# Optimization experiments

Measured on AMD Instinct MI355X. Metric: run time of the kernel, lower is better.

The kernel has to match this reference:

```python
import jax, jax.numpy as jnp
import numpy as np

EPS = 1e-12  # matches torch F.normalize default eps
TEMP = 0.1


def _gram(x):
    # L2-normalize rows; for unit vectors 1 - 0.5*||xi-xj||^2 == xi . xj
    n = x / jnp.maximum(jnp.linalg.norm(x, axis=-1, keepdims=True), EPS)
    return n @ n.T  # [N, N]


def setup_inputs() -> dict:
    key = jax.random.key(0)
    k1, k2, k3, k4 = jax.random.split(key, 4)
    N, D = 4096, 512
    return {
        "fm_rgb": jax.random.normal(k1, (N, D), dtype=jnp.float32),
        "fm_depth": jax.random.normal(k2, (N, D), dtype=jnp.float32),
        "fm_ir": jax.random.normal(k3, (N, D), dtype=jnp.float32),
        "fm_t": jax.random.normal(k4, (N, D), dtype=jnp.float32),
    }


def reference(fm_rgb, fm_depth, fm_ir, fm_t):
    G_rgb = _gram(fm_rgb)
    G_depth = _gram(fm_depth)
    G_ir = _gram(fm_ir)
    G_t = _gram(fm_t)
    inv_t = 1.0 / TEMP
    loss_rgb = jnp.mean((G_t * inv_t - G_rgb * inv_t) ** 2)
    loss_depth = jnp.mean((G_t * inv_t - G_depth * inv_t) ** 2)
    loss_ir = jnp.mean((G_t * inv_t - G_ir * inv_t) ** 2)
    return loss_rgb + loss_depth + loss_ir
```

## Files before the change

kernel.cpp:

```cpp
#include <hip/hip_runtime.h>
#include <hip/hip_bf16.h>


typedef __attribute__((ext_vector_type(4))) float floatx4;
typedef __attribute__((ext_vector_type(8))) unsigned short ushort8;

#define N_ROWS 4096
#define DDIM   512
#define NT8_BYTES    ((size_t)4 * DDIM * N_ROWS)
#define SLICE_FLOATS ((size_t)112 * 16384)
#define NSPLIT 4
#define LOSS_SCALE 9.094947017729282e-11f

__device__ __forceinline__ const float* sel_mod(int mod, const float* a,
                                                const float* b, const float* c,
                                                const float* d) {
  return mod == 0 ? a : mod == 1 ? b : mod == 2 ? c : d;
}

__global__ __launch_bounds__(256) void preprocess_kernel(
    const float* __restrict__ in0, const float* __restrict__ in1,
    const float* __restrict__ in2, const float* __restrict__ in3,
    unsigned char* __restrict__ nT8) {
  int mod = blockIdx.y;
  int k0 = blockIdx.x * 64;
  const float* X = sel_mod(mod, in0, in1, in2, in3) + (size_t)k0 * DDIM;

  __shared__ float rsc[64];
  __shared__ unsigned short tile[128][72];

  int t = threadIdx.x;
  int w = t >> 6, lane = t & 63;

#pragma unroll
  for (int i = 0; i < 16; ++i) {
    int r = w * 16 + i;
    const float4* rp = (const float4*)(X + (size_t)r * DDIM);
    float4 a = rp[lane];
    float4 b = rp[lane + 64];
    float ss = a.x * a.x + a.y * a.y + a.z * a.z + a.w * a.w +
               b.x * b.x + b.y * b.y + b.z * b.z + b.w * b.w;
#pragma unroll
    for (int off = 32; off > 0; off >>= 1) ss += __shfl_down(ss, off, 64);
    if (lane == 0) rsc[r] = 16.0f / fmaxf(sqrtf(ss), 1e-12f);
  }
  __syncthreads();

  for (int p = 0; p < 4; ++p) {
#pragma unroll
    for (int it = 0; it < 8; ++it) {
      int idx = it * 256 + t;
      int r = idx >> 5;
      int c4 = idx & 31;
      float4 v = ((const float4*)(X + (size_t)r * DDIM + p * 128))[c4];
      float sc = rsc[r];
      __hip_bfloat16 h0 = __float2bfloat16(v.x * sc);
      __hip_bfloat16 h1 = __float2bfloat16(v.y * sc);
      __hip_bfloat16 h2 = __float2bfloat16(v.z * sc);
      __hip_bfloat16 h3 = __float2bfloat16(v.w * sc);
      tile[c4 * 4 + 0][r] = *(unsigned short*)&h0;
      tile[c4 * 4 + 1][r] = *(unsigned short*)&h1;
      tile[c4 * 4 + 2][r] = *(unsigned short*)&h2;
      tile[c4 * 4 + 3][r] = *(unsigned short*)&h3;
    }
    __syncthreads();
#pragma unroll
    for (int it = 0; it < 2; ++it) {
      int idx = it * 256 + t;
      int c = idx >> 2;
      int g = idx & 3;
      ushort8 u0 = *(const ushort8*)&tile[c][g * 16];
      ushort8 u1 = *(const ushort8*)&tile[c][g * 16 + 8];
      float f[16];
#pragma unroll
      for (int j = 0; j < 8; ++j) {
        f[j] = __uint_as_float(((unsigned int)(unsigned short)u0[j]) << 16);
        f[8 + j] = __uint_as_float(((unsigned int)(unsigned short)u1[j]) << 16);
      }
      unsigned int wds[4];
#pragma unroll
      for (int q = 0; q < 4; ++q) {
        unsigned int pk = __builtin_amdgcn_cvt_pk_fp8_f32(f[4 * q], f[4 * q + 1], 0, 0);
        pk = __builtin_amdgcn_cvt_pk_fp8_f32(f[4 * q + 2], f[4 * q + 3], pk, 1);
        wds[q] = pk;
      }
      uint4 out = {wds[0], wds[1], wds[2], wds[3]};
      *(uint4*)(nT8 + ((size_t)(mod * DDIM + p * 128 + c)) * N_ROWS + k0 +
                g * 16) = out;
    }
    __syncthreads();
  }
}

__device__ __forceinline__ void stage_tiles(
    const unsigned char* __restrict__ Abase,
    const unsigned char* __restrict__ Bbase, int k0,
    unsigned char* lsA, unsigned char* lsB, int wave, int lane) {
  int rr = lane >> 3;
  int s = lane & 7;
#pragma unroll
  for (int c = 0; c < 4; ++c) {
    int base = wave * 32 + c * 8;
    int row = base + rr;
    int gc = s ^ ((row >> 1) & 7);
    const unsigned char* ga = Abase + (size_t)row * N_ROWS + k0 + gc * 16;
    const unsigned char* gb = Bbase + (size_t)row * N_ROWS + k0 + gc * 16;
    __builtin_amdgcn_global_load_lds(
        (__attribute__((address_space(1))) void*)(void*)ga,
        (__attribute__((address_space(3))) void*)(void*)&lsA[base * 128],
        16, 0, 0);
    __builtin_amdgcn_global_load_lds(
        (__attribute__((address_space(1))) void*)(void*)gb,
        (__attribute__((address_space(3))) void*)(void*)&lsB[base * 128],
        16, 0, 0);
  }
}

__device__ __forceinline__ void compute_tiles(
    const unsigned char* lsA, const unsigned char* lsB,
    floatx4 acc[4][4], int wr, int wc, int lm, int lq) {
#pragma unroll
  for (int ks = 0; ks < 4; ++ks) {
    int j = ks * 4 + lq;
    int cg = j >> 1;
    int sub = (j & 1) * 8;
    long long af[4], bf[4];
#pragma unroll
    for (int mi = 0; mi < 4; ++mi) {
      int row = wr + mi * 16 + lm;
      int slot = cg ^ ((row >> 1) & 7);
      af[mi] = *(const long long*)&lsA[row * 128 + slot * 16 + sub];
    }
#pragma unroll
    for (int ni = 0; ni < 4; ++ni) {
      int row = wc + ni * 16 + lm;
      int slot = cg ^ ((row >> 1) & 7);
      bf[ni] = *(const long long*)&lsB[row * 128 + slot * 16 + sub];
    }
#pragma unroll
    for (int mi = 0; mi < 4; ++mi)
#pragma unroll
      for (int ni = 0; ni < 4; ++ni)
        acc[mi][ni] = __builtin_amdgcn_mfma_f32_16x16x32_fp8_fp8(
            af[mi], bf[ni], acc[mi][ni], 0, 0, 0);
  }
}

__global__ __launch_bounds__(256) void gram_frob_kernel(
    const unsigned char* __restrict__ nT8, float* __restrict__ Cbuf) {
  __shared__ unsigned char ls[2][2][128 * 128];

  const int pa[7] = {3, 0, 1, 2, 3, 3, 3};
  const int pb[7] = {3, 0, 1, 2, 0, 1, 2};

  int tile = blockIdx.x;
  int prod = blockIdx.y;
  int kbase = blockIdx.z * 1024;
  int a0 = (tile >> 2) * 128;
  int b0 = (tile & 3) * 128;
  const unsigned char* Abase = nT8 + ((size_t)pa[prod] * DDIM + a0) * N_ROWS;
  const unsigned char* Bbase = nT8 + ((size_t)pb[prod] * DDIM + b0) * N_ROWS;

  int t = threadIdx.x;
  int wave = t >> 6;
  int lane = t & 63;
  int wr = (wave >> 1) * 64;
  int wc = (wave & 1) * 64;
  int lm = lane & 15;
  int lq = lane >> 4;

  floatx4 zero = {0.f, 0.f, 0.f, 0.f};
  floatx4 acc[4][4];
#pragma unroll
  for (int mi = 0; mi < 4; ++mi)
#pragma unroll
    for (int ni = 0; ni < 4; ++ni) acc[mi][ni] = zero;

  stage_tiles(Abase, Bbase, kbase, ls[0][0], ls[0][1], wave, lane);
  __syncthreads();
  int k0 = kbase + 128;
  for (int i = 0; i < 3; ++i) {
    stage_tiles(Abase, Bbase, k0, ls[1][0], ls[1][1], wave, lane);
    compute_tiles(ls[0][0], ls[0][1], acc, wr, wc, lm, lq);
    __syncthreads();
    stage_tiles(Abase, Bbase, k0 + 128, ls[0][0], ls[0][1], wave, lane);
    compute_tiles(ls[1][0], ls[1][1], acc, wr, wc, lm, lq);
    __syncthreads();
    k0 += 256;
  }
  stage_tiles(Abase, Bbase, kbase + 896, ls[1][0], ls[1][1], wave, lane);
  compute_tiles(ls[0][0], ls[0][1], acc, wr, wc, lm, lq);
  __syncthreads();
  compute_tiles(ls[1][0], ls[1][1], acc, wr, wc, lm, lq);

  float* Cp = Cbuf + (size_t)blockIdx.z * SLICE_FLOATS +
              (size_t)(prod * 16 + tile) * 16384;
#pragma unroll
  for (int mi = 0; mi < 4; ++mi)
#pragma unroll
    for (int ni = 0; ni < 4; ++ni) {
      int j = mi * 4 + ni;
      *(floatx4*)(Cp + (size_t)(j * 256 + t) * 4) = acc[mi][ni];
    }
}

__global__ __launch_bounds__(256) void reduce_kernel(
    const float4* __restrict__ Cbuf, float* __restrict__ out) {
  const float w[7] = {3.f, 1.f, 1.f, 1.f, -2.f, -2.f, -2.f};
  const size_t S4 = SLICE_FLOATS / 4;
  int t = threadIdx.x;
  float s = 0.f;
  size_t stride = (size_t)gridDim.x * 256;
  for (size_t i = (size_t)blockIdx.x * 256 + t; i < S4; i += stride) {
    float4 a = Cbuf[i];
    float4 b = Cbuf[i + S4];
    float4 c = Cbuf[i + 2 * S4];
    float4 d = Cbuf[i + 3 * S4];
    float vx = a.x + b.x + c.x + d.x;
    float vy = a.y + b.y + c.y + d.y;
    float vz = a.z + b.z + c.z + d.z;
    float vw = a.w + b.w + c.w + d.w;
    float ww = w[i >> 16];
    s += ww * (vx * vx + vy * vy + vz * vz + vw * vw);
  }
#pragma unroll
  for (int off = 32; off > 0; off >>= 1) s += __shfl_down(s, off, 64);
  __shared__ float red[4];
  if ((t & 63) == 0) red[t >> 6] = s;
  __syncthreads();
  if (t == 0)
    atomicAdd(out, LOSS_SCALE * (red[0] + red[1] + red[2] + red[3]));
}

extern "C" void kernel_launch(void* const* d_in, const int* in_sizes, int n_in,
                              void* d_out, int out_size, void* d_ws, size_t ws_size,
                              hipStream_t stream) {
  const float* in_rgb   = (const float*)d_in[0];
  const float* in_depth = (const float*)d_in[1];
  const float* in_ir    = (const float*)d_in[2];
  const float* in_t     = (const float*)d_in[3];

  unsigned char* nT8 = (unsigned char*)d_ws;
  float* Cbuf = (float*)((char*)d_ws + NT8_BYTES);

  hipMemsetAsync(d_out, 0, out_size * sizeof(float), stream);

  preprocess_kernel<<<dim3(64, 4), 256, 0, stream>>>(in_rgb, in_depth, in_ir,
                                                     in_t, nT8);
  gram_frob_kernel<<<dim3(16, 7, NSPLIT), 256, 0, stream>>>(nT8, Cbuf);
  reduce_kernel<<<448, 256, 0, stream>>>((const float4*)Cbuf, (float*)d_out);
}
```

Before: 120.3 us.

## Drop split-K and fuse Frobenius reduction into gram kernel epilogue

Removes the split-K partitioning, so each block accumulates the full K=4096 dot products itself and squares and reduces its tile in registers before one weighted atomicAdd. This eliminates the large Cbuf partial-product workspace write, the separate reduce kernel, and the memset, which now happens inside the preprocess kernel. Blocks grow to 512 threads with 8 waves, each computing a 64x32 sub-tile, and LDS fragments are loaded as 16-byte vectors up front. The trade-off is only 112 blocks on a GPU with many more CUs, each running a longer K loop, which risks underutilising the device.

```diff
diff --git a/kernel.cpp b/kernel.cpp
--- a/kernel.cpp
+++ b/kernel.cpp
@@ -4,12 +4,10 @@
 
 typedef __attribute__((ext_vector_type(4))) float floatx4;
 typedef __attribute__((ext_vector_type(8))) unsigned short ushort8;
+typedef __attribute__((ext_vector_type(2))) long long llx2;
 
 #define N_ROWS 4096
 #define DDIM   512
-#define NT8_BYTES    ((size_t)4 * DDIM * N_ROWS)
-#define SLICE_FLOATS ((size_t)112 * 16384)
-#define NSPLIT 4
 #define LOSS_SCALE 9.094947017729282e-11f
 
 __device__ __forceinline__ const float* sel_mod(int mod, const float* a,
@@ -21,10 +19,13 @@
 __global__ __launch_bounds__(256) void preprocess_kernel(
     const float* __restrict__ in0, const float* __restrict__ in1,
     const float* __restrict__ in2, const float* __restrict__ in3,
-    unsigned char* __restrict__ nT8) {
+    unsigned char* __restrict__ nT8, float* __restrict__ out) {
   int mod = blockIdx.y;
   int k0 = blockIdx.x * 64;
   const float* X = sel_mod(mod, in0, in1, in2, in3) + (size_t)k0 * DDIM;
+
+  if (blockIdx.x == 0 && blockIdx.y == 0 && threadIdx.x == 0)
+    out[0] = 0.f;
 
   __shared__ float rsc[64];
   __shared__ unsigned short tile[128][72];
@@ -80,13 +81,14 @@
       unsigned int wds[4];
 #pragma unroll
       for (int q = 0; q < 4; ++q) {
-        unsigned int pk = __builtin_amdgcn_cvt_pk_fp8_f32(f[4 * q], f[4 * q + 1], 0, 0);
+        unsigned int pk =
+            __builtin_amdgcn_cvt_pk_fp8_f32(f[4 * q], f[4 * q + 1], 0, 0);
         pk = __builtin_amdgcn_cvt_pk_fp8_f32(f[4 * q + 2], f[4 * q + 3], pk, 1);
         wds[q] = pk;
       }
-      uint4 out = {wds[0], wds[1], wds[2], wds[3]};
+      uint4 o = {wds[0], wds[1], wds[2], wds[3]};
       *(uint4*)(nT8 + ((size_t)(mod * DDIM + p * 128 + c)) * N_ROWS + k0 +
-                g * 16) = out;
+                g * 16) = o;
     }
     __syncthreads();
   }
@@ -95,12 +97,12 @@
 __device__ __forceinline__ void stage_tiles(
     const unsigned char* __restrict__ Abase,
     const unsigned char* __restrict__ Bbase, int k0,
-    unsigned char* lsA, unsigned char* lsB, int wave, int lane) {
+    unsigned char* lsA, unsigned char* lsB, int w, int lane) {
   int rr = lane >> 3;
   int s = lane & 7;
 #pragma unroll
-  for (int c = 0; c < 4; ++c) {
-    int base = wave * 32 + c * 8;
+  for (int c = 0; c < 2; ++c) {
+    int base = w * 16 + c * 8;
     int row = base + rr;
     int gc = s ^ ((row >> 1) & 7);
     const unsigned char* ga = Abase + (size_t)row * N_ROWS + k0 + gc * 16;
@@ -118,118 +120,100 @@
 
 __device__ __forceinline__ void compute_tiles(
     const unsigned char* lsA, const unsigned char* lsB,
-    floatx4 acc[4][4], int wr, int wc, int lm, int lq) {
+    floatx4 acc[4][2], int wr, int wc, int lm, int lq) {
+  llx2 A16[4][2], B16[2][2];
+#pragma unroll
+  for (int mi = 0; mi < 4; ++mi) {
+    int row = wr + mi * 16 + lm;
+    int sw = (row >> 1) & 7;
+    A16[mi][0] = *(const llx2*)&lsA[row * 128 + ((lq * 2) ^ sw) * 16];
+    A16[mi][1] = *(const llx2*)&lsA[row * 128 + ((lq * 2 + 1) ^ sw) * 16];
+  }
+#pragma unroll
+  for (int ni = 0; ni < 2; ++ni) {
+    int row = wc + ni * 16 + lm;
+    int sw = (row >> 1) & 7;
+    B16[ni][0] = *(const llx2*)&lsB[row * 128 + ((lq * 2) ^ sw) * 16];
+    B16[ni][1] = *(const llx2*)&lsB[row * 128 + ((lq * 2 + 1) ^ sw) * 16];
+  }
 #pragma unroll
   for (int ks = 0; ks < 4; ++ks) {
-    int j = ks * 4 + lq;
-    int cg = j >> 1;
-    int sub = (j & 1) * 8;
-    long long af[4], bf[4];
-#pragma unroll
-    for (int mi = 0; mi < 4; ++mi) {
-      int row = wr + mi * 16 + lm;
-      int slot = cg ^ ((row >> 1) & 7);
-      af[mi] = *(const long long*)&lsA[row * 128 + slot * 16 + sub];
-    }
-#pragma unroll
-    for (int ni = 0; ni < 4; ++ni) {
-      int row = wc + ni * 16 + lm;
-      int slot = cg ^ ((row >> 1) & 7);
-      bf[ni] = *(const long long*)&lsB[row * 128 + slot * 16 + sub];
-    }
+    int h = ks >> 1, e = ks & 1;
 #pragma unroll
     for (int mi = 0; mi < 4; ++mi)
 #pragma unroll
-      for (int ni = 0; ni < 4; ++ni)
+      for (int ni = 0; ni < 2; ++ni)
         acc[mi][ni] = __builtin_amdgcn_mfma_f32_16x16x32_fp8_fp8(
-            af[mi], bf[ni], acc[mi][ni], 0, 0, 0);
-  }
-}
-
-__global__ __launch_bounds__(256) void gram_frob_kernel(
-    const unsigned char* __restrict__ nT8, float* __restrict__ Cbuf) {
+            A16[mi][h][e], B16[ni][h][e], acc[mi][ni], 0, 0, 0);
+  }
+}
+
+__global__ __launch_bounds__(512) void gram_frob_kernel(
+    const unsigned char* __restrict__ nT8, float* __restrict__ out) {
   __shared__ unsigned char ls[2][2][128 * 128];
-
-  const int pa[7] = {3, 0, 1, 2, 3, 3, 3};
-  const int pb[7] = {3, 0, 1, 2, 0, 1, 2};
+  __shared__ float red[8];
+
+  const int   pa[7] = {3, 0, 1, 2, 3, 3, 3};
+  const int   pb[7] = {3, 0, 1, 2, 0, 1, 2};
+  const float pw[7] = {3.f, 1.f, 1.f, 1.f, -2.f, -2.f, -2.f};
 
   int tile = blockIdx.x;
   int prod = blockIdx.y;
-  int kbase = blockIdx.z * 1024;
   int a0 = (tile >> 2) * 128;
   int b0 = (tile & 3) * 128;
   const unsigned char* Abase = nT8 + ((size_t)pa[prod] * DDIM + a0) * N_ROWS;
   const unsigned char* Bbase = nT8 + ((size_t)pb[prod] * DDIM + b0) * N_ROWS;
 
   int t = threadIdx.x;
-  int wave = t >> 6;
+  int w = t >> 6;
   int lane = t & 63;
-  int wr = (wave >> 1) * 64;
-  int wc = (wave & 1) * 64;
+  int wr = (w >> 2) * 64;
+  int wc = (w & 3) * 32;
   int lm = lane & 15;
   int lq = lane >> 4;
 
   floatx4 zero = {0.f, 0.f, 0.f, 0.f};
-  floatx4 acc[4][4];
+  floatx4 acc[4][2];
 #pragma unroll
   for (int mi = 0; mi < 4; ++mi)
 #pragma unroll
-    for (int ni = 0; ni < 4; ++ni) acc[mi][ni] = zero;
-
-  stage_tiles(Abase, Bbase, kbase, ls[0][0], ls[0][1], wave, lane);
-  __syncthreads();
-  int k0 = kbase + 128;
-  for (int i = 0; i < 3; ++i) {
-    stage_tiles(Abase, Bbase, k0, ls[1][0], ls[1][1], wave, lane);
+    for (int ni = 0; ni < 2; ++ni) acc[mi][ni] = zero;
+
+  stage_tiles(Abase, Bbase, 0, ls[0][0], ls[0][1], w, lane);
+  __syncthreads();
+  for (int i = 0; i < 15; ++i) {
+    int k0 = (2 * i + 1) * 128;
+    stage_tiles(Abase, Bbase, k0, ls[1][0], ls[1][1], w, lane);
     compute_tiles(ls[0][0], ls[0][1], acc, wr, wc, lm, lq);
     __syncthreads();
-    stage_tiles(Abase, Bbase, k0 + 128, ls[0][0], ls[0][1], wave, lane);
+    stage_tiles(Abase, Bbase, k0 + 128, ls[0][0], ls[0][1], w, lane);
     compute_tiles(ls[1][0], ls[1][1], acc, wr, wc, lm, lq);
     __syncthreads();
-    k0 += 256;
-  }
-  stage_tiles(Abase, Bbase, kbase + 896, ls[1][0], ls[1][1], wave, lane);
+  }
+  stage_tiles(Abase, Bbase, 31 * 128, ls[1][0], ls[1][1], w, lane);
   compute_tiles(ls[0][0], ls[0][1], acc, wr, wc, lm, lq);
   __syncthreads();
   compute_tiles(ls[1][0], ls[1][1], acc, wr, wc, lm, lq);
 
-  float* Cp = Cbuf + (size_t)blockIdx.z * SLICE_FLOATS +
-              (size_t)(prod * 16 + tile) * 16384;
+  float s = 0.f;
 #pragma unroll
   for (int mi = 0; mi < 4; ++mi)
 #pragma unroll
-    for (int ni = 0; ni < 4; ++ni) {
-      int j = mi * 4 + ni;
-      *(floatx4*)(Cp + (size_t)(j * 256 + t) * 4) = acc[mi][ni];
-    }
-}
-
-__global__ __launch_bounds__(256) void reduce_kernel(
-    const float4* __restrict__ Cbuf, float* __restrict__ out) {
-  const float w[7] = {3.f, 1.f, 1.f, 1.f, -2.f, -2.f, -2.f};
-  const size_t S4 = SLICE_FLOATS / 4;
-  int t = threadIdx.x;
-  float s = 0.f;
-  size_t stride = (size_t)gridDim.x * 256;
-  for (size_t i = (size_t)blockIdx.x * 256 + t; i < S4; i += stride) {
-    float4 a = Cbuf[i];
-    float4 b = Cbuf[i + S4];
-    float4 c = Cbuf[i + 2 * S4];
-    float4 d = Cbuf[i + 3 * S4];
-    float vx = a.x + b.x + c.x + d.x;
-    float vy = a.y + b.y + c.y + d.y;
-    float vz = a.z + b.z + c.z + d.z;
-    float vw = a.w + b.w + c.w + d.w;
-    float ww = w[i >> 16];
-    s += ww * (vx * vx + vy * vy + vz * vz + vw * vw);
-  }
+    for (int ni = 0; ni < 2; ++ni)
+#pragma unroll
+      for (int r = 0; r < 4; ++r) {
+        float v = acc[mi][ni][r];
+        s += v * v;
+      }
 #pragma unroll
   for (int off = 32; off > 0; off >>= 1) s += __shfl_down(s, off, 64);
-  __shared__ float red[4];
-  if ((t & 63) == 0) red[t >> 6] = s;
-  __syncthreads();
-  if (t == 0)
-    atomicAdd(out, LOSS_SCALE * (red[0] + red[1] + red[2] + red[3]));
+  if (lane == 0) red[w] = s;
+  __syncthreads();
+  if (t == 0) {
+    float tot = red[0] + red[1] + red[2] + red[3] + red[4] + red[5] + red[6] +
+                red[7];
+    atomicAdd(out, pw[prod] * LOSS_SCALE * tot);
+  }
 }
 
 extern "C" void kernel_launch(void* const* d_in, const int* in_sizes, int n_in,
@@ -241,12 +225,8 @@
   const float* in_t     = (const float*)d_in[3];
 
   unsigned char* nT8 = (unsigned char*)d_ws;
-  float* Cbuf = (float*)((char*)d_ws + NT8_BYTES);
-
-  hipMemsetAsync(d_out, 0, out_size * sizeof(float), stream);
-
-  preprocess_kernel<<<dim3(64, 4), 256, 0, stream>>>(in_rgb, in_depth, in_ir,
-                                                     in_t, nT8);
-  gram_frob_kernel<<<dim3(16, 7, NSPLIT), 256, 0, stream>>>(nT8, Cbuf);
-  reduce_kernel<<<448, 256, 0, stream>>>((const float4*)Cbuf, (float*)d_out);
-}
+
+  preprocess_kernel<<<dim3(64, 4), 256, 0, stream>>>(
+      in_rgb, in_depth, in_ir, in_t, nT8, (float*)d_out);
+  gram_frob_kernel<<<dim3(16, 7), 512, 0, stream>>>(nT8, (float*)d_out);
+}
```

New measurement: 124.7 us. 3.7% more time.
